# Performance work log

Measured on AMD Instinct MI355X. Metric: run time of the kernel, lower is better.

## Reference

```python
import jax, jax.numpy as jnp
import numpy as np

WS = (7, 7)          # window size
NUM_HEADS = 4
DIM = 128
B_ = 4096            # batch * num_windows
NW = 256             # num windows per image (mask leading dim)
N = WS[0] * WS[1]    # 49 tokens per window


def _relative_position_index(ws):
    coords = np.stack(np.meshgrid(np.arange(ws[0]), np.arange(ws[1]), indexing='ij'))
    coords = coords.reshape(2, -1)                      # [2, N]
    rel = coords[:, :, None] - coords[:, None, :]       # [2, N, N]
    rel = rel.transpose(1, 2, 0).astype(np.int64)       # [N, N, 2]
    rel[:, :, 0] += ws[0] - 1
    rel[:, :, 1] += ws[1] - 1
    rel[:, :, 0] *= 2 * ws[1] - 1
    return rel.sum(-1)                                  # [N, N] in [0, (2w-1)^2)

REL_POS_INDEX = jnp.asarray(_relative_position_index(WS))


def setup_inputs() -> dict:
    key = jax.random.key(0)
    ks = jax.random.split(key, 4)
    x = jax.random.normal(ks[0], (B_, N, DIM), dtype=jnp.float32)
    mask = jnp.zeros((NW, N, N), dtype=jnp.float32)
    qkv_w = jax.random.normal(ks[1], (DIM, 3 * DIM), dtype=jnp.float32) * 0.02
    qkv_b = jnp.zeros((3 * DIM,), dtype=jnp.float32)
    proj_w = jax.random.normal(ks[2], (DIM, DIM), dtype=jnp.float32) * 0.02
    proj_b = jnp.zeros((DIM,), dtype=jnp.float32)
    bias_table = jax.random.normal(ks[3], ((2 * WS[0] - 1) * (2 * WS[1] - 1), NUM_HEADS), dtype=jnp.float32) * 0.02
    return {"x": x, "mask": mask, "qkv_w": qkv_w, "qkv_b": qkv_b,
            "proj_w": proj_w, "proj_b": proj_b, "bias_table": bias_table}


def reference(x, mask, qkv_w, qkv_b, proj_w, proj_b, bias_table):
    B, n, C = x.shape
    H = NUM_HEADS
    hd = C // H
    scale = hd ** (-0.5)

    qkv = x @ qkv_w + qkv_b                            # [B, N, 3C]
    qkv = qkv.reshape(B, n, 3, H, hd).transpose(2, 0, 3, 1, 4)  # [3, B, H, N, hd]
    q, k, v = qkv[0], qkv[1], qkv[2]

    attn = jnp.einsum('bhnd,bhmd->bhnm', q * scale, k)  # [B, H, N, N]

    # gathered relative-position bias: [N*N, H] -> [H, N, N]
    bias = bias_table[REL_POS_INDEX.reshape(-1)].reshape(n, n, H).transpose(2, 0, 1)
    attn = attn + bias[None]

    nW = mask.shape[0]
    attn = attn.reshape(-1, nW, H, n, n) + mask[None, :, None].astype(attn.dtype)
    attn = attn.reshape(-1, H, n, n)
    attn = jax.nn.softmax(attn, axis=-1)

    out = jnp.einsum('bhnm,bhmd->bnhd', attn, v).reshape(B, n, C)
    out = out @ proj_w + proj_b
    return out
```

## Files before the change

### kernel.cpp

```cpp
#include <hip/hip_runtime.h>
#include <hip/hip_bf16.h>


typedef __attribute__((ext_vector_type(8))) short bf16x8;
typedef __attribute__((ext_vector_type(4))) float f32x4;
typedef unsigned long long ull;

#define NTOK  49
#define CDIM  128
#define NWIN  256
#define SCALE 0.17677669529663687f
#define PROJ_WOFF 49152
#define WB_BYTES  131072

static __device__ __forceinline__ unsigned pk2(float a, float b) {
    __hip_bfloat162 h = __float22bfloat162_rn(make_float2(a, b));
    unsigned u; __builtin_memcpy(&u, &h, 4); return u;
}
static __device__ __forceinline__ short bf1(float a) {
    __hip_bfloat16 h = __float2bfloat16(a);
    unsigned short u; __builtin_memcpy(&u, &h, 2); return (short)u;
}
static __device__ __forceinline__ bf16x8 repack(unsigned p00, unsigned p01,
                                                unsigned p10, unsigned p11,
                                                int src0, int src1, bool hi) {
    union { bf16x8 v; unsigned u[4]; } t;
    unsigned a0, a1;
    a0 = __shfl((int)p00, src0, 64); a1 = __shfl((int)p10, src0, 64); t.u[0] = hi ? a1 : a0;
    a0 = __shfl((int)p01, src0, 64); a1 = __shfl((int)p11, src0, 64); t.u[1] = hi ? a1 : a0;
    a0 = __shfl((int)p00, src1, 64); a1 = __shfl((int)p10, src1, 64); t.u[2] = hi ? a1 : a0;
    a0 = __shfl((int)p01, src1, 64); a1 = __shfl((int)p11, src1, 64); t.u[3] = hi ? a1 : a0;
    return t.v;
}

__global__ void prep_w(const float* __restrict__ qkv_w,
                       const float* __restrict__ proj_w,
                       short* __restrict__ wb) {
    const int fid = blockIdx.x;
    const int l   = threadIdx.x;
    const int lq = l & 15, lg = l >> 4;
    bf16x8 v;
    if (fid < 96) {
        const int nt = fid >> 2, kk = fid & 3;
        const float s = (fid < 32) ? SCALE : 1.0f;
        #pragma unroll
        for (int j = 0; j < 8; ++j)
            v[j] = bf1(qkv_w[(kk*32 + lg*8 + j)*384 + nt*16 + lq] * s);
        *(bf16x8*)(wb + fid*512 + l*8) = v;
    } else {
        const int f2 = fid - 96;
        const int nt = f2 >> 2, kk = f2 & 3;
        #pragma unroll
        for (int j = 0; j < 8; ++j)
            v[j] = bf1(proj_w[(kk*32 + lg*8 + j)*128 + nt*16 + lq]);
        *(bf16x8*)(wb + PROJ_WOFF + f2*512 + l*8) = v;
    }
}

__global__ void prep_bm(const float* __restrict__ mask,
                        const float* __restrict__ bias_table,
                        ull* __restrict__ bm) {
    const int win = blockIdx.x;
    const int tid = threadIdx.x;
    const int l = tid & 63, wave = tid >> 6;
    const int lq = l & 15, lg = l >> 4;
    const int qtok = wave*16 + lq;
    const float* mwin = mask + (size_t)win * (NTOK * NTOK);
    const unsigned NEG = pk2(-1e30f, -1e30f);
    ull* dst = bm + (((size_t)win*4 + wave)*16)*64 + l;
    #pragma unroll
    for (int nt = 0; nt < 4; ++nt)
        #pragma unroll
        for (int r = 0; r < 4; ++r) {
            unsigned w0 = NEG, w1 = NEG;
            const int kt = nt*16 + lg*4 + r;
            if (qtok < NTOK && kt < NTOK) {
                const int ridx = (qtok/7 - kt/7 + 6)*13 + (qtok%7 - kt%7 + 6);
                const f32x4 b4 = *(const f32x4*)(bias_table + ridx*4);
                const float mv = mwin[qtok*NTOK + kt];
                w0 = pk2(b4[0] + mv, b4[1] + mv);
                w1 = pk2(b4[2] + mv, b4[3] + mv);
            }
            dst[(nt*4 + r)*64] = (ull)w0 | ((ull)w1 << 32);
        }
}

__global__ __launch_bounds__(256, 4)
void win_attn(const float* __restrict__ x,
              const float* __restrict__ mask,
              const float* __restrict__ qkv_b,
              const float* __restrict__ proj_b,
              const float* __restrict__ bias_table,
              const short* __restrict__ wb,
              const ull* __restrict__ bmt,
              float* __restrict__ out) {
    __shared__ __align__(16) short kl[64 * 128];
    __shared__ __align__(16) short vt[128 * 64];

    const int b    = blockIdx.x;
    const int tid  = threadIdx.x;
    const int l    = tid & 63;
    const int wave = tid >> 6;
    const int lq   = l & 15, lg = l >> 4;
    const int m0   = wave * 16;
    const int qtok = m0 + lq;

    const float* xb = x + (size_t)b * (NTOK * CDIM);
    bf16x8 xa[4];
    {
        int row = qtok; if (row > 48) row = 48;
        const float* pr = xb + row*CDIM + lg*8;
        #pragma unroll
        for (int kk = 0; kk < 4; ++kk) {
            float4 f0 = *(const float4*)(pr + kk*32);
            float4 f1 = *(const float4*)(pr + kk*32 + 4);
            union { bf16x8 v; unsigned u[4]; } t;
            t.u[0] = pk2(f0.x, f0.y);
            t.u[1] = pk2(f0.z, f0.w);
            t.u[2] = pk2(f1.x, f1.y);
            t.u[3] = pk2(f1.z, f1.w);
            xa[kk] = t.v;
        }
    }

    unsigned qpk[8][2];
    #pragma unroll
    for (int np = 0; np < 12; ++np) {
        const int n0 = 2*np, n1 = 2*np + 1;
        bf16x8 wfA[4], wfB[4];
        #pragma unroll
        for (int kk = 0; kk < 4; ++kk)
            wfA[kk] = *(const bf16x8*)(wb + (n0*4 + kk)*512 + l*8);
        #pragma unroll
        for (int kk = 0; kk < 4; ++kk)
            wfB[kk] = *(const bf16x8*)(wb + (n1*4 + kk)*512 + l*8);
        f32x4 aA = *(const f32x4*)(qkv_b + n0*16 + lg*4);
        f32x4 aB = *(const f32x4*)(qkv_b + n1*16 + lg*4);
        if (n0 < 8) { aA = aA * SCALE; aB = aB * SCALE; }
        #pragma unroll
        for (int kk = 0; kk < 4; ++kk)
            aA = __builtin_amdgcn_mfma_f32_16x16x32_bf16(wfA[kk], xa[kk], aA, 0, 0, 0);
        #pragma unroll
        for (int kk = 0; kk < 4; ++kk)
            aB = __builtin_amdgcn_mfma_f32_16x16x32_bf16(wfB[kk], xa[kk], aB, 0, 0, 0);
        #pragma unroll
        for (int e = 0; e < 2; ++e) {
            const int nt = 2*np + e;
            const f32x4 acc = e ? aB : aA;
            if (nt < 8) {
                qpk[nt][0] = pk2(acc[0], acc[1]);
                qpk[nt][1] = pk2(acc[2], acc[3]);
            } else if (nt < 16) {
                unsigned w0 = pk2(acc[0], acc[1]);
                unsigned w1 = pk2(acc[2], acc[3]);
                const int ub  = (nt - 8)*2 + (lg >> 1);
                const int off = qtok*128 + ((ub ^ (qtok & 7)) << 3) + (lg & 1)*4;
                *(ull*)(kl + off) = (ull)w0 | ((ull)w1 << 32);
            } else {
                #pragma unroll
                for (int r = 0; r < 4; ++r) {
                    const int dim = (nt - 16)*16 + lg*4 + r;
                    vt[dim*64 + (((qtok >> 3) ^ (dim & 7)) << 3) + (qtok & 7)] = bf1(acc[r]);
                }
            }
        }
    }

    unsigned bmpk[4][4][2];
    if (bmt) {
        const ull* src = bmt + ((((size_t)(b & (NWIN-1)))*4 + wave)*16)*64 + l;
        #pragma unroll
        for (int nt = 0; nt < 4; ++nt)
            #pragma unroll
            for (int r = 0; r < 4; ++r) {
                const ull u = src[(nt*4 + r)*64];
                bmpk[nt][r][0] = (unsigned)u;
                bmpk[nt][r][1] = (unsigned)(u >> 32);
            }
    } else {
        const float* mwin = mask + (size_t)(b & (NWIN - 1)) * (NTOK * NTOK);
        const unsigned NEG = pk2(-1e30f, -1e30f);
        #pragma unroll
        for (int nt = 0; nt < 4; ++nt)
            #pragma unroll
            for (int r = 0; r < 4; ++r) {
                const int kt = nt*16 + lg*4 + r;
                if (qtok < NTOK && kt < NTOK) {
                    const int ridx = (qtok/7 - kt/7 + 6)*13 + (qtok%7 - kt%7 + 6);
                    const f32x4 b4 = *(const f32x4*)(bias_table + ridx*4);
                    const float mv = mwin[qtok*NTOK + kt];
                    bmpk[nt][r][0] = pk2(b4[0] + mv, b4[1] + mv);
                    bmpk[nt][r][1] = pk2(b4[2] + mv, b4[3] + mv);
                } else {
                    bmpk[nt][r][0] = NEG; bmpk[nt][r][1] = NEG;
                }
            }
    }
    __syncthreads();

    const int src0 = lq + 16*((2*lg + 0) & 3);
    const int src1 = lq + 16*((2*lg + 1) & 3);
    const bool hi  = (lg >> 1);
    unsigned aopk[8][2];

    #pragma unroll
    for (int hp = 0; hp < 2; ++hp) {
        const int h0 = 2*hp, h1 = h0 + 1;
        const bf16x8 qfA = repack(qpk[2*h0][0], qpk[2*h0][1], qpk[2*h0+1][0], qpk[2*h0+1][1],
                                  src0, src1, hi);
        const bf16x8 qfB = repack(qpk[2*h1][0], qpk[2*h1][1], qpk[2*h1+1][0], qpk[2*h1+1][1],
                                  src0, src1, hi);
        f32x4 sA[4], sB[4];
        __builtin_amdgcn_s_setprio(1);
        #pragma unroll
        for (int nt = 0; nt < 4; ++nt) {
            const int krow = nt*16 + lq;
            bf16x8 kfA = *(const bf16x8*)(kl + krow*128 + (((h0*4 + lg) ^ (krow & 7)) << 3));
            bf16x8 kfB = *(const bf16x8*)(kl + krow*128 + (((h1*4 + lg) ^ (krow & 7)) << 3));
            f32x4 z = {0.f, 0.f, 0.f, 0.f};
            sA[nt] = __builtin_amdgcn_mfma_f32_16x16x32_bf16(kfA, qfA, z, 0, 0, 0);
            sB[nt] = __builtin_amdgcn_mfma_f32_16x16x32_bf16(kfB, qfB, z, 0, 0, 0);
        }
        __builtin_amdgcn_s_setprio(0);
        #pragma unroll
        for (int nt = 0; nt < 4; ++nt)
            #pragma unroll
            for (int r = 0; r < 4; ++r) {
                const unsigned u = bmpk[nt][r][hp];
                sA[nt][r] += __uint_as_float(u << 16);
                sB[nt][r] += __uint_as_float(u & 0xffff0000u);
            }
        float sumA, sumB;
        {
            float a_[4], b_[4];
            #pragma unroll
            for (int nt = 0; nt < 4; ++nt) {
                #pragma unroll
                for (int r = 0; r < 4; ++r) {
                    sA[nt][r] = __expf(sA[nt][r]);
                    sB[nt][r] = __expf(sB[nt][r]);
                }
                a_[nt] = (sA[nt][0] + sA[nt][1]) + (sA[nt][2] + sA[nt][3]);
                b_[nt] = (sB[nt][0] + sB[nt][1]) + (sB[nt][2] + sB[nt][3]);
            }
            sumA = (a_[0] + a_[1]) + (a_[2] + a_[3]);
            sumB = (b_[0] + b_[1]) + (b_[2] + b_[3]);
        }
        sumA += __shfl_xor(sumA, 16, 64);
        sumB += __shfl_xor(sumB, 16, 64);
        sumA += __shfl_xor(sumA, 32, 64);
        sumB += __shfl_xor(sumB, 32, 64);
        const float invA = 1.0f / sumA;
        const float invB = 1.0f / sumB;
        unsigned pkvA[4][2], pkvB[4][2];
        #pragma unroll
        for (int nt = 0; nt < 4; ++nt) {
            pkvA[nt][0] = pk2(sA[nt][0]*invA, sA[nt][1]*invA);
            pkvA[nt][1] = pk2(sA[nt][2]*invA, sA[nt][3]*invA);
            pkvB[nt][0] = pk2(sB[nt][0]*invB, sB[nt][1]*invB);
            pkvB[nt][1] = pk2(sB[nt][2]*invB, sB[nt][3]*invB);
        }
        bf16x8 paA[2], paB[2];
        #pragma unroll
        for (int c = 0; c < 2; ++c) {
            paA[c] = repack(pkvA[2*c][0], pkvA[2*c][1], pkvA[2*c+1][0], pkvA[2*c+1][1],
                            src0, src1, hi);
            paB[c] = repack(pkvB[2*c][0], pkvB[2*c][1], pkvB[2*c+1][0], pkvB[2*c+1][1],
                            src0, src1, hi);
        }
        #pragma unroll
        for (int dn = 0; dn < 2; ++dn) {
            f32x4 oA = {0.f, 0.f, 0.f, 0.f};
            f32x4 oB = {0.f, 0.f, 0.f, 0.f};
            __builtin_amdgcn_s_setprio(1);
            #pragma unroll
            for (int kk = 0; kk < 2; ++kk) {
                const int dimA = h0*32 + dn*16 + lq;
                const int dimB = h1*32 + dn*16 + lq;
                bf16x8 vfA = *(const bf16x8*)(vt + dimA*64 + (((kk*4 + lg) ^ (dimA & 7)) << 3));
                bf16x8 vfB = *(const bf16x8*)(vt + dimB*64 + (((kk*4 + lg) ^ (dimB & 7)) << 3));
                oA = __builtin_amdgcn_mfma_f32_16x16x32_bf16(vfA, paA[kk], oA, 0, 0, 0);
                oB = __builtin_amdgcn_mfma_f32_16x16x32_bf16(vfB, paB[kk], oB, 0, 0, 0);
            }
            __builtin_amdgcn_s_setprio(0);
            aopk[2*h0 + dn][0] = pk2(oA[0], oA[1]);
            aopk[2*h0 + dn][1] = pk2(oA[2], oA[3]);
            aopk[2*h1 + dn][0] = pk2(oB[0], oB[1]);
            aopk[2*h1 + dn][1] = pk2(oB[2], oB[3]);
        }
    }

    bf16x8 ab[4];
    #pragma unroll
    for (int kk = 0; kk < 4; ++kk)
        ab[kk] = repack(aopk[2*kk][0], aopk[2*kk][1], aopk[2*kk+1][0], aopk[2*kk+1][1],
                        src0, src1, hi);
    float* ob = out + (size_t)b * (NTOK * CDIM);
    #pragma unroll
    for (int nt = 0; nt < 8; ++nt) {
        bf16x8 wf[4];
        #pragma unroll
        for (int kk = 0; kk < 4; ++kk)
            wf[kk] = *(const bf16x8*)(wb + PROJ_WOFF + (nt*4 + kk)*512 + l*8);
        f32x4 acc = *(const f32x4*)(proj_b + nt*16 + lg*4);
        #pragma unroll
        for (int kk = 0; kk < 4; ++kk)
            acc = __builtin_amdgcn_mfma_f32_16x16x32_bf16(wf[kk], ab[kk], acc, 0, 0, 0);
        if (qtok < NTOK)
            *(f32x4*)(ob + qtok*CDIM + nt*16 + lg*4) = acc;
    }
}

extern "C" void kernel_launch(void* const* d_in, const int* in_sizes, int n_in,
                              void* d_out, int out_size, void* d_ws, size_t ws_size,
                              hipStream_t stream) {
    (void)in_sizes; (void)n_in; (void)out_size;
    const float* x          = (const float*)d_in[0];
    const float* mask       = (const float*)d_in[1];
    const float* qkv_w      = (const float*)d_in[2];
    const float* qkv_b      = (const float*)d_in[3];
    const float* proj_w     = (const float*)d_in[4];
    const float* proj_b     = (const float*)d_in[5];
    const float* bias_table = (const float*)d_in[6];
    float* out = (float*)d_out;
    short* wb  = (short*)d_ws;

    const size_t bm_bytes = (size_t)NWIN * 4 * 16 * 64 * 8;
    ull* bmt = nullptr;
    if (ws_size >= (size_t)WB_BYTES + bm_bytes)
        bmt = (ull*)((char*)d_ws + WB_BYTES);

    hipLaunchKernelGGL(prep_w, dim3(128), dim3(64), 0, stream, qkv_w, proj_w, wb);
    if (bmt)
        hipLaunchKernelGGL(prep_bm, dim3(NWIN), dim3(256), 0, stream, mask, bias_table, bmt);
    hipLaunchKernelGGL(win_attn, dim3(4096), dim3(256), 0, stream,
                       x, mask, qkv_b, proj_b, bias_table, wb, bmt, out);
}
```

Baseline: 125.2 us.

## Stage QKV and projection weight tiles cooperatively through LDS

Instead of each wave loading its own full copy of the bf16 weight fragments from global memory, the block now loads each pair of 16-column weight tiles once with one 16-byte load per thread into a shared LDS buffer. All four waves then read their fragments from there. This targets the redundant global/L2 traffic of four waves fetching the same weights. In exchange it adds an 8 KB LDS buffer, which may reduce occupancy, and two block barriers per tile step across 12 QKV and 4 projection steps, which serialize the waves. The existing barrier before attention is folded into the loop's trailing barrier.

```diff
diff --git a/kernel.cpp b/kernel.cpp
--- a/kernel.cpp
+++ b/kernel.cpp
@@ -96,6 +96,7 @@
               float* __restrict__ out) {
     __shared__ __align__(16) short kl[64 * 128];
     __shared__ __align__(16) short vt[128 * 64];
+    __shared__ __align__(16) short wls[4096];
 
     const int b    = blockIdx.x;
     const int tid  = threadIdx.x;
@@ -126,14 +127,20 @@
     unsigned qpk[8][2];
     #pragma unroll
     for (int np = 0; np < 12; ++np) {
-        const int n0 = 2*np, n1 = 2*np + 1;
+        const int n0 = 2*np, n1 = n0 + 1;
+        {
+            bf16x8 s0 = *(const bf16x8*)(wb + np*4096 + tid*8);
+            bf16x8 s1 = *(const bf16x8*)(wb + np*4096 + 2048 + tid*8);
+            *(bf16x8*)(wls + tid*8)        = s0;
+            *(bf16x8*)(wls + 2048 + tid*8) = s1;
+        }
+        __syncthreads();
         bf16x8 wfA[4], wfB[4];
         #pragma unroll
-        for (int kk = 0; kk < 4; ++kk)
-            wfA[kk] = *(const bf16x8*)(wb + (n0*4 + kk)*512 + l*8);
-        #pragma unroll
-        for (int kk = 0; kk < 4; ++kk)
-            wfB[kk] = *(const bf16x8*)(wb + (n1*4 + kk)*512 + l*8);
+        for (int kk = 0; kk < 4; ++kk) {
+            wfA[kk] = *(const bf16x8*)(wls + kk*512 + l*8);
+            wfB[kk] = *(const bf16x8*)(wls + 2048 + kk*512 + l*8);
+        }
         f32x4 aA = *(const f32x4*)(qkv_b + n0*16 + lg*4);
         f32x4 aB = *(const f32x4*)(qkv_b + n1*16 + lg*4);
         if (n0 < 8) { aA = aA * SCALE; aB = aB * SCALE; }
@@ -164,6 +171,7 @@
                 }
             }
         }
+        __syncthreads();
     }
 
     unsigned bmpk[4][4][2];
@@ -196,7 +204,6 @@
                 }
             }
     }
-    __syncthreads();
 
     const int src0 = lq + 16*((2*lg + 0) & 3);
     const int src1 = lq + 16*((2*lg + 1) & 3);
@@ -297,17 +304,27 @@
                         src0, src1, hi);
     float* ob = out + (size_t)b * (NTOK * CDIM);
     #pragma unroll
-    for (int nt = 0; nt < 8; ++nt) {
-        bf16x8 wf[4];
-        #pragma unroll
-        for (int kk = 0; kk < 4; ++kk)
-            wf[kk] = *(const bf16x8*)(wb + PROJ_WOFF + (nt*4 + kk)*512 + l*8);
-        f32x4 acc = *(const f32x4*)(proj_b + nt*16 + lg*4);
-        #pragma unroll
-        for (int kk = 0; kk < 4; ++kk)
-            acc = __builtin_amdgcn_mfma_f32_16x16x32_bf16(wf[kk], ab[kk], acc, 0, 0, 0);
-        if (qtok < NTOK)
-            *(f32x4*)(ob + qtok*CDIM + nt*16 + lg*4) = acc;
+    for (int nc = 0; nc < 4; ++nc) {
+        bf16x8 s0 = *(const bf16x8*)(wb + PROJ_WOFF + nc*4096 + tid*8);
+        bf16x8 s1 = *(const bf16x8*)(wb + PROJ_WOFF + nc*4096 + 2048 + tid*8);
+        __syncthreads();
+        *(bf16x8*)(wls + tid*8)        = s0;
+        *(bf16x8*)(wls + 2048 + tid*8) = s1;
+        __syncthreads();
+        #pragma unroll
+        for (int e = 0; e < 2; ++e) {
+            const int nt = nc*2 + e;
+            bf16x8 wf[4];
+            #pragma unroll
+            for (int kk = 0; kk < 4; ++kk)
+                wf[kk] = *(const bf16x8*)(wls + e*2048 + kk*512 + l*8);
+            f32x4 acc = *(const f32x4*)(proj_b + nt*16 + lg*4);
+            #pragma unroll
+            for (int kk = 0; kk < 4; ++kk)
+                acc = __builtin_amdgcn_mfma_f32_16x16x32_bf16(wf[kk], ab[kk], acc, 0, 0, 0);
+            if (qtok < NTOK)
+                *(f32x4*)(ob + qtok*CDIM + nt*16 + lg*4) = acc;
+        }
     }
 }
 
```

Result: faster. 117.1 us (-6.5%).

## Stage weight tiles in LDS via double-buffered global_load_lds

Applied to the files above, without the earlier changes.

Previously every wave loaded the same QKV and projection weight fragments directly from global memory. Now the block cooperatively copies each 4 KB weight tile into an LDS double buffer with global_load_lds, prefetching the next tile while the current one feeds the MFMAs. This cuts redundant global/L2 traffic fourfold, at the cost of a __syncthreads per tile (32 barriers), extra LDS that may reduce occupancy, and losing the previous two-tile interleaving of independent MFMA chains.

```diff
diff --git a/kernel.cpp b/kernel.cpp
--- a/kernel.cpp
+++ b/kernel.cpp
@@ -20,6 +20,12 @@
 static __device__ __forceinline__ short bf1(float a) {
     __hip_bfloat16 h = __float2bfloat16(a);
     unsigned short u; __builtin_memcpy(&u, &h, 2); return (short)u;
+}
+static __device__ __forceinline__ void gll16(const short* gsrc, short* ldst) {
+    __builtin_amdgcn_global_load_lds(
+        (const __attribute__((address_space(1))) unsigned*)(const void*)gsrc,
+        (__attribute__((address_space(3))) unsigned*)(void*)ldst,
+        16, 0, 0);
 }
 static __device__ __forceinline__ bf16x8 repack(unsigned p00, unsigned p01,
                                                 unsigned p10, unsigned p11,
@@ -96,6 +102,7 @@
               float* __restrict__ out) {
     __shared__ __align__(16) short kl[64 * 128];
     __shared__ __align__(16) short vt[128 * 64];
+    __shared__ __align__(16) short wls[4096];
 
     const int b    = blockIdx.x;
     const int tid  = threadIdx.x;
@@ -104,6 +111,8 @@
     const int lq   = l & 15, lg = l >> 4;
     const int m0   = wave * 16;
     const int qtok = m0 + lq;
+
+    gll16(wb + tid*8, wls + wave*512);
 
     const float* xb = x + (size_t)b * (NTOK * CDIM);
     bf16x8 xa[4];
@@ -122,48 +131,42 @@
             xa[kk] = t.v;
         }
     }
+    __syncthreads();
 
     unsigned qpk[8][2];
     #pragma unroll
-    for (int np = 0; np < 12; ++np) {
-        const int n0 = 2*np, n1 = 2*np + 1;
-        bf16x8 wfA[4], wfB[4];
+    for (int nt = 0; nt < 24; ++nt) {
+        short* cur = wls + ((nt & 1) ? 2048 : 0);
+        if (nt < 23) {
+            short* oth = wls + ((nt & 1) ? 0 : 2048);
+            gll16(wb + (nt + 1)*2048 + tid*8, oth + wave*512);
+        }
+        bf16x8 wf[4];
         #pragma unroll
         for (int kk = 0; kk < 4; ++kk)
-            wfA[kk] = *(const bf16x8*)(wb + (n0*4 + kk)*512 + l*8);
+            wf[kk] = *(const bf16x8*)(cur + kk*512 + l*8);
+        f32x4 acc = *(const f32x4*)(qkv_b + nt*16 + lg*4);
+        if (nt < 8) acc = acc * SCALE;
         #pragma unroll
         for (int kk = 0; kk < 4; ++kk)
-            wfB[kk] = *(const bf16x8*)(wb + (n1*4 + kk)*512 + l*8);
-        f32x4 aA = *(const f32x4*)(qkv_b + n0*16 + lg*4);
-        f32x4 aB = *(const f32x4*)(qkv_b + n1*16 + lg*4);
-        if (n0 < 8) { aA = aA * SCALE; aB = aB * SCALE; }
-        #pragma unroll
-        for (int kk = 0; kk < 4; ++kk)
-            aA = __builtin_amdgcn_mfma_f32_16x16x32_bf16(wfA[kk], xa[kk], aA, 0, 0, 0);
-        #pragma unroll
-        for (int kk = 0; kk < 4; ++kk)
-            aB = __builtin_amdgcn_mfma_f32_16x16x32_bf16(wfB[kk], xa[kk], aB, 0, 0, 0);
-        #pragma unroll
-        for (int e = 0; e < 2; ++e) {
-            const int nt = 2*np + e;
-            const f32x4 acc = e ? aB : aA;
-            if (nt < 8) {
-                qpk[nt][0] = pk2(acc[0], acc[1]);
-                qpk[nt][1] = pk2(acc[2], acc[3]);
-            } else if (nt < 16) {
-                unsigned w0 = pk2(acc[0], acc[1]);
-                unsigned w1 = pk2(acc[2], acc[3]);
-                const int ub  = (nt - 8)*2 + (lg >> 1);
-                const int off = qtok*128 + ((ub ^ (qtok & 7)) << 3) + (lg & 1)*4;
-                *(ull*)(kl + off) = (ull)w0 | ((ull)w1 << 32);
-            } else {
-                #pragma unroll
-                for (int r = 0; r < 4; ++r) {
-                    const int dim = (nt - 16)*16 + lg*4 + r;
-                    vt[dim*64 + (((qtok >> 3) ^ (dim & 7)) << 3) + (qtok & 7)] = bf1(acc[r]);
-                }
-            }
-        }
+            acc = __builtin_amdgcn_mfma_f32_16x16x32_bf16(wf[kk], xa[kk], acc, 0, 0, 0);
+        if (nt < 8) {
+            qpk[nt][0] = pk2(acc[0], acc[1]);
+            qpk[nt][1] = pk2(acc[2], acc[3]);
+        } else if (nt < 16) {
+            unsigned w0 = pk2(acc[0], acc[1]);
+            unsigned w1 = pk2(acc[2], acc[3]);
+            const int ub  = (nt - 8)*2 + (lg >> 1);
+            const int off = qtok*128 + ((ub ^ (qtok & 7)) << 3) + (lg & 1)*4;
+            *(ull*)(kl + off) = (ull)w0 | ((ull)w1 << 32);
+        } else {
+            #pragma unroll
+            for (int r = 0; r < 4; ++r) {
+                const int dim = (nt - 16)*16 + lg*4 + r;
+                vt[dim*64 + (((qtok >> 3) ^ (dim & 7)) << 3) + (qtok & 7)] = bf1(acc[r]);
+            }
+        }
+        __syncthreads();
     }
 
     unsigned bmpk[4][4][2];
@@ -196,7 +199,8 @@
                 }
             }
     }
-    __syncthreads();
+
+    gll16(wb + PROJ_WOFF + tid*8, wls + wave*512);
 
     const int src0 = lq + 16*((2*lg + 0) & 3);
     const int src1 = lq + 16*((2*lg + 1) & 3);
@@ -296,18 +300,25 @@
         ab[kk] = repack(aopk[2*kk][0], aopk[2*kk][1], aopk[2*kk+1][0], aopk[2*kk+1][1],
                         src0, src1, hi);
     float* ob = out + (size_t)b * (NTOK * CDIM);
+    __syncthreads();
     #pragma unroll
     for (int nt = 0; nt < 8; ++nt) {
+        short* cur = wls + ((nt & 1) ? 2048 : 0);
+        if (nt < 7) {
+            short* oth = wls + ((nt & 1) ? 0 : 2048);
+            gll16(wb + PROJ_WOFF + (nt + 1)*2048 + tid*8, oth + wave*512);
+        }
         bf16x8 wf[4];
         #pragma unroll
         for (int kk = 0; kk < 4; ++kk)
-            wf[kk] = *(const bf16x8*)(wb + PROJ_WOFF + (nt*4 + kk)*512 + l*8);
+            wf[kk] = *(const bf16x8*)(cur + kk*512 + l*8);
         f32x4 acc = *(const f32x4*)(proj_b + nt*16 + lg*4);
         #pragma unroll
         for (int kk = 0; kk < 4; ++kk)
             acc = __builtin_amdgcn_mfma_f32_16x16x32_bf16(wf[kk], ab[kk], acc, 0, 0, 0);
         if (qtok < NTOK)
             *(f32x4*)(ob + qtok*CDIM + nt*16 + lg*4) = acc;
+        if (nt < 7) __syncthreads();
     }
 }
 
```

After: 126.5 us. About the same (+1.1%).

## Process two windows per block and stage shared weights through LDS double buffer

Applied to the files above, without the earlier changes.

Each 512-thread block now handles two windows, and the QKV and projection weight fragments are loaded cooperatively into a double-buffered LDS tile, with register prefetch of the next chunk. Before, every wave read its weight fragments straight from global/L2 memory. The goal is to halve the global weight traffic per window and hide load latency. In exchange there are many more block-wide barriers, LDS use roughly doubles (about 80KB per block), and launch_bounds(512,4) may limit occupancy or force register spilling.

```diff
diff --git a/kernel.cpp b/kernel.cpp
--- a/kernel.cpp
+++ b/kernel.cpp
@@ -85,7 +85,7 @@
         }
 }
 
-__global__ __launch_bounds__(256, 4)
+__global__ __launch_bounds__(512, 4)
 void win_attn(const float* __restrict__ x,
               const float* __restrict__ mask,
               const float* __restrict__ qkv_b,
@@ -94,16 +94,25 @@
               const short* __restrict__ wb,
               const ull* __restrict__ bmt,
               float* __restrict__ out) {
-    __shared__ __align__(16) short kl[64 * 128];
-    __shared__ __align__(16) short vt[128 * 64];
-
-    const int b    = blockIdx.x;
+    __shared__ __align__(16) short kl[2 * 64 * 128];
+    __shared__ __align__(16) short vt[2 * 128 * 64];
+    __shared__ __align__(16) short wls[8192];
+
     const int tid  = threadIdx.x;
     const int l    = tid & 63;
-    const int wave = tid >> 6;
+    const int w8   = tid >> 6;
+    const int win  = w8 >> 2;
+    const int wave = w8 & 3;
     const int lq   = l & 15, lg = l >> 4;
     const int m0   = wave * 16;
     const int qtok = m0 + lq;
+    const int b    = blockIdx.x * 2 + win;
+
+    short* klw = kl + win * 8192;
+    short* vtw = vt + win * 8192;
+
+    bf16x8 rE = *(const bf16x8*)(wb + 0*4096 + tid*8);
+    bf16x8 rO = *(const bf16x8*)(wb + 1*4096 + tid*8);
 
     const float* xb = x + (size_t)b * (NTOK * CDIM);
     bf16x8 xa[4];
@@ -122,31 +131,30 @@
             xa[kk] = t.v;
         }
     }
+    *(bf16x8*)(wls + tid*8) = rE;
+    __syncthreads();
 
     unsigned qpk[8][2];
     #pragma unroll
     for (int np = 0; np < 12; ++np) {
-        const int n0 = 2*np, n1 = 2*np + 1;
-        bf16x8 wfA[4], wfB[4];
-        #pragma unroll
-        for (int kk = 0; kk < 4; ++kk)
-            wfA[kk] = *(const bf16x8*)(wb + (n0*4 + kk)*512 + l*8);
-        #pragma unroll
-        for (int kk = 0; kk < 4; ++kk)
-            wfB[kk] = *(const bf16x8*)(wb + (n1*4 + kk)*512 + l*8);
-        f32x4 aA = *(const f32x4*)(qkv_b + n0*16 + lg*4);
-        f32x4 aB = *(const f32x4*)(qkv_b + n1*16 + lg*4);
-        if (n0 < 8) { aA = aA * SCALE; aB = aB * SCALE; }
-        #pragma unroll
-        for (int kk = 0; kk < 4; ++kk)
-            aA = __builtin_amdgcn_mfma_f32_16x16x32_bf16(wfA[kk], xa[kk], aA, 0, 0, 0);
-        #pragma unroll
-        for (int kk = 0; kk < 4; ++kk)
-            aB = __builtin_amdgcn_mfma_f32_16x16x32_bf16(wfB[kk], xa[kk], aB, 0, 0, 0);
+        short* cur = wls + ((np & 1) ? 4096 : 0);
+        short* oth = wls + ((np & 1) ? 0 : 4096);
+        if (np + 2 < 12) {
+            if ((np & 1) == 0) rE = *(const bf16x8*)(wb + (np + 2)*4096 + tid*8);
+            else               rO = *(const bf16x8*)(wb + (np + 2)*4096 + tid*8);
+        }
         #pragma unroll
         for (int e = 0; e < 2; ++e) {
             const int nt = 2*np + e;
-            const f32x4 acc = e ? aB : aA;
+            bf16x8 wf[4];
+            #pragma unroll
+            for (int kk = 0; kk < 4; ++kk)
+                wf[kk] = *(const bf16x8*)(cur + e*2048 + kk*512 + l*8);
+            f32x4 acc = *(const f32x4*)(qkv_b + nt*16 + lg*4);
+            if (nt < 8) acc = acc * SCALE;
+            #pragma unroll
+            for (int kk = 0; kk < 4; ++kk)
+                acc = __builtin_amdgcn_mfma_f32_16x16x32_bf16(wf[kk], xa[kk], acc, 0, 0, 0);
             if (nt < 8) {
                 qpk[nt][0] = pk2(acc[0], acc[1]);
                 qpk[nt][1] = pk2(acc[2], acc[3]);
@@ -155,15 +163,18 @@
                 unsigned w1 = pk2(acc[2], acc[3]);
                 const int ub  = (nt - 8)*2 + (lg >> 1);
                 const int off = qtok*128 + ((ub ^ (qtok & 7)) << 3) + (lg & 1)*4;
-                *(ull*)(kl + off) = (ull)w0 | ((ull)w1 << 32);
+                *(ull*)(klw + off) = (ull)w0 | ((ull)w1 << 32);
             } else {
                 #pragma unroll
                 for (int r = 0; r < 4; ++r) {
                     const int dim = (nt - 16)*16 + lg*4 + r;
-                    vt[dim*64 + (((qtok >> 3) ^ (dim & 7)) << 3) + (qtok & 7)] = bf1(acc[r]);
+                    vtw[dim*64 + (((qtok >> 3) ^ (dim & 7)) << 3) + (qtok & 7)] = bf1(acc[r]);
                 }
             }
         }
+        if (np + 1 < 12)
+            *(bf16x8*)(oth + tid*8) = ((np & 1) == 0) ? rO : rE;
+        __syncthreads();
     }
 
     unsigned bmpk[4][4][2];
@@ -196,7 +207,6 @@
                 }
             }
     }
-    __syncthreads();
 
     const int src0 = lq + 16*((2*lg + 0) & 3);
     const int src1 = lq + 16*((2*lg + 1) & 3);
@@ -215,8 +225,8 @@
         #pragma unroll
         for (int nt = 0; nt < 4; ++nt) {
             const int krow = nt*16 + lq;
-            bf16x8 kfA = *(const bf16x8*)(kl + krow*128 + (((h0*4 + lg) ^ (krow & 7)) << 3));
-            bf16x8 kfB = *(const bf16x8*)(kl + krow*128 + (((h1*4 + lg) ^ (krow & 7)) << 3));
+            bf16x8 kfA = *(const bf16x8*)(klw + krow*128 + (((h0*4 + lg) ^ (krow & 7)) << 3));
+            bf16x8 kfB = *(const bf16x8*)(klw + krow*128 + (((h1*4 + lg) ^ (krow & 7)) << 3));
             f32x4 z = {0.f, 0.f, 0.f, 0.f};
             sA[nt] = __builtin_amdgcn_mfma_f32_16x16x32_bf16(kfA, qfA, z, 0, 0, 0);
             sB[nt] = __builtin_amdgcn_mfma_f32_16x16x32_bf16(kfB, qfB, z, 0, 0, 0);
@@ -277,8 +287,8 @@
             for (int kk = 0; kk < 2; ++kk) {
                 const int dimA = h0*32 + dn*16 + lq;
                 const int dimB = h1*32 + dn*16 + lq;
-                bf16x8 vfA = *(const bf16x8*)(vt + dimA*64 + (((kk*4 + lg) ^ (dimA & 7)) << 3));
-                bf16x8 vfB = *(const bf16x8*)(vt + dimB*64 + (((kk*4 + lg) ^ (dimB & 7)) << 3));
+                bf16x8 vfA = *(const bf16x8*)(vtw + dimA*64 + (((kk*4 + lg) ^ (dimA & 7)) << 3));
+                bf16x8 vfB = *(const bf16x8*)(vtw + dimB*64 + (((kk*4 + lg) ^ (dimB & 7)) << 3));
                 oA = __builtin_amdgcn_mfma_f32_16x16x32_bf16(vfA, paA[kk], oA, 0, 0, 0);
                 oB = __builtin_amdgcn_mfma_f32_16x16x32_bf16(vfB, paB[kk], oB, 0, 0, 0);
             }
@@ -290,24 +300,41 @@
         }
     }
 
+    bf16x8 pE = *(const bf16x8*)(wb + PROJ_WOFF + 0*4096 + tid*8);
+    bf16x8 pO = *(const bf16x8*)(wb + PROJ_WOFF + 1*4096 + tid*8);
     bf16x8 ab[4];
     #pragma unroll
     for (int kk = 0; kk < 4; ++kk)
         ab[kk] = repack(aopk[2*kk][0], aopk[2*kk][1], aopk[2*kk+1][0], aopk[2*kk+1][1],
                         src0, src1, hi);
     float* ob = out + (size_t)b * (NTOK * CDIM);
-    #pragma unroll
-    for (int nt = 0; nt < 8; ++nt) {
-        bf16x8 wf[4];
-        #pragma unroll
-        for (int kk = 0; kk < 4; ++kk)
-            wf[kk] = *(const bf16x8*)(wb + PROJ_WOFF + (nt*4 + kk)*512 + l*8);
-        f32x4 acc = *(const f32x4*)(proj_b + nt*16 + lg*4);
-        #pragma unroll
-        for (int kk = 0; kk < 4; ++kk)
-            acc = __builtin_amdgcn_mfma_f32_16x16x32_bf16(wf[kk], ab[kk], acc, 0, 0, 0);
-        if (qtok < NTOK)
-            *(f32x4*)(ob + qtok*CDIM + nt*16 + lg*4) = acc;
+    *(bf16x8*)(wls + tid*8) = pE;
+    __syncthreads();
+    #pragma unroll
+    for (int np = 0; np < 4; ++np) {
+        short* cur = wls + ((np & 1) ? 4096 : 0);
+        short* oth = wls + ((np & 1) ? 0 : 4096);
+        if (np + 2 < 4) {
+            if ((np & 1) == 0) pE = *(const bf16x8*)(wb + PROJ_WOFF + (np + 2)*4096 + tid*8);
+            else               pO = *(const bf16x8*)(wb + PROJ_WOFF + (np + 2)*4096 + tid*8);
+        }
+        #pragma unroll
+        for (int e = 0; e < 2; ++e) {
+            const int nt = 2*np + e;
+            bf16x8 wf[4];
+            #pragma unroll
+            for (int kk = 0; kk < 4; ++kk)
+                wf[kk] = *(const bf16x8*)(cur + e*2048 + kk*512 + l*8);
+            f32x4 acc = *(const f32x4*)(proj_b + nt*16 + lg*4);
+            #pragma unroll
+            for (int kk = 0; kk < 4; ++kk)
+                acc = __builtin_amdgcn_mfma_f32_16x16x32_bf16(wf[kk], ab[kk], acc, 0, 0, 0);
+            if (qtok < NTOK)
+                *(f32x4*)(ob + qtok*CDIM + nt*16 + lg*4) = acc;
+        }
+        if (np + 1 < 4)
+            *(bf16x8*)(oth + tid*8) = ((np & 1) == 0) ? pO : pE;
+        if (np < 3) __syncthreads();
     }
 }
 
@@ -333,6 +360,6 @@
     hipLaunchKernelGGL(prep_w, dim3(128), dim3(64), 0, stream, qkv_w, proj_w, wb);
     if (bmt)
         hipLaunchKernelGGL(prep_bm, dim3(NWIN), dim3(256), 0, stream, mask, bias_table, bmt);
-    hipLaunchKernelGGL(win_attn, dim3(4096), dim3(256), 0, stream,
+    hipLaunchKernelGGL(win_attn, dim3(2048), dim3(512), 0, stream,
                        x, mask, qkv_b, proj_b, bias_table, wb, bmt, out);
 }
```

Measured after the change: 116.5 us. 1.07x faster.
